# Performance work log

Hardware: AMD Instinct MI355X
Metric: run time of the kernel (lower is better)

## Reference

```python
import jax, jax.numpy as jnp
import numpy as np

B, L, N, C, H, COND = 2, 8, 256, 1024, 16, 64
D = C // H  # 64, divisible by 4


def setup_inputs() -> dict:
    key = jax.random.key(0)
    ks = jax.random.split(key, 16)
    w = lambda k, i, o: (jax.random.normal(k, (i, o), jnp.float32) / np.sqrt(i)).astype(jnp.float32)
    return {
        "s_frames": jax.random.normal(ks[0], (B, L, N, C), jnp.float32),
        "frame_idx": jnp.arange(L, dtype=jnp.int32),
        "seq_idx": jnp.sort(jax.random.randint(ks[1], (B, N), 0, 1024), axis=-1).astype(jnp.int32),
        "mask": jax.random.randint(ks[2], (B, L, N), 0, 2).astype(jnp.int32),
        "cond": jax.random.normal(ks[3], (B, COND), jnp.float32),
        "W_ada": w(ks[4], COND, 2 * C), "b_ada": jnp.zeros((2 * C,), jnp.float32),
        "Wq": w(ks[5], C, C), "bq": jnp.zeros((C,), jnp.float32),
        "Wk": w(ks[6], C, C), "bk": jnp.zeros((C,), jnp.float32),
        "Wv": w(ks[7], C, C), "bv": jnp.zeros((C,), jnp.float32),
        "Wo": w(ks[8], C, C), "bo": jnp.zeros((C,), jnp.float32),
    }


def _rope2d(x, pos_s, pos_f, inv_freq):
    # x: [B,H,T,D]; first half of D rotated by residue positions, second half by frame positions.
    half = x.shape[-1] // 2
    quarter = half // 2

    def rot(xh, pos):  # xh [B,H,T,half], pos [B,T]
        ang = pos[:, None, :, None] * inv_freq  # [B,1,T,quarter]
        c, s = jnp.cos(ang), jnp.sin(ang)
        x1, x2 = xh[..., :quarter], xh[..., quarter:]
        return jnp.concatenate([x1 * c - x2 * s, x1 * s + x2 * c], axis=-1)

    return jnp.concatenate([rot(x[..., :half], pos_s), rot(x[..., half:], pos_f)], axis=-1)


def reference(s_frames, frame_idx, seq_idx, mask, cond,
              W_ada, b_ada, Wq, bq, Wk, bk, Wv, bv, Wo, bo):
    Bx, Lx, Nx, Cx = s_frames.shape
    T = Lx * Nx
    Dh = Cx // H
    scale = Dh ** (-0.5)

    # AdaLN: LayerNorm (no affine) then conditional scale/shift from cond
    mu = s_frames.mean(-1, keepdims=True)
    var = ((s_frames - mu) ** 2).mean(-1, keepdims=True)
    xn = (s_frames - mu) * jax.lax.rsqrt(var + 1e-5)
    ss = cond @ W_ada + b_ada                      # [B, 2C]
    shift, sc = ss[:, :Cx], ss[:, Cx:]
    x = xn * (1.0 + sc[:, None, None, :]) + shift[:, None, None, :]

    xf = x.reshape(Bx, T, Cx)
    split = lambda t: t.reshape(Bx, T, H, Dh).transpose(0, 2, 1, 3)  # [B,H,T,D]
    q = split(xf @ Wq + bq)
    k = split(xf @ Wk + bk)
    v = split(xf @ Wv + bv)

    # 2D RoPE positions (token t = l*N + n)
    half = Dh // 2
    quarter = half // 2
    inv_freq = 1.0 / (10000.0 ** (jnp.arange(quarter, dtype=jnp.float32) * 2.0 / half))
    pos_s = jnp.tile(seq_idx, (1, Lx)).astype(jnp.float32)                                  # [B,T]
    pos_f = jnp.broadcast_to(jnp.repeat(frame_idx, Nx).astype(jnp.float32)[None], (Bx, T))  # [B,T]
    q = _rope2d(q, pos_s, pos_f, inv_freq)
    k = _rope2d(k, pos_s, pos_f, inv_freq)

    # additive bias: block-causal over frames + key padding mask
    fi = jnp.repeat(jnp.arange(Lx), Nx)                      # [T]
    future = fi[None, :] > fi[:, None]                       # [T,T] key frame > query frame
    bias = jnp.where(future, -jnp.inf, 0.0)[None, None]      # [1,1,T,T]
    pad = (mask.reshape(Bx, T) == 0)
    bias = jnp.where(pad[:, None, None, :], -jnp.inf, bias)  # [B,1,T,T]

    logits = jnp.einsum('bhtd,bhsd->bhts', q, k) * scale + bias
    w = jax.nn.softmax(logits, axis=-1)
    out = jnp.einsum('bhts,bhsd->bhtd', w, v)
    out = out.transpose(0, 2, 1, 3).reshape(Bx, Lx, Nx, Cx)
    return out @ Wo + bo
```

## Files before the change

kernel.cpp:

```cpp
#include <hip/hip_runtime.h>

typedef __bf16 bf16;
typedef __bf16 bf16x8 __attribute__((ext_vector_type(8)));
typedef __bf16 bf16x4 __attribute__((ext_vector_type(4)));
typedef float  f32x4  __attribute__((ext_vector_type(4)));

#define B_ 2
#define L_ 8
#define N_ 256
#define C_ 1024
#define H_ 16
#define D_ 64
#define T_ 2048
#define M_ 4096
#define COND_ 64

#define QSCALE 0.18033688011111372f

__device__ __forceinline__ void gload_lds16(const void* g, void* lds) {
  __builtin_amdgcn_global_load_lds((const __attribute__((address_space(1))) void*)g,
                                   (__attribute__((address_space(3))) void*)lds, 16, 0, 0);
}

__global__ __launch_bounds__(256) void k_ada(const float* __restrict__ cond,
                                             const float* __restrict__ W,
                                             const float* __restrict__ ba,
                                             float* __restrict__ ss) {
  int j = blockIdx.x * 256 + threadIdx.x;
  int b = j >> 11;
  int n = j & 2047;
  float s = ba[n];
  #pragma unroll
  for (int i = 0; i < COND_; ++i) s += cond[b * COND_ + i] * W[i * 2048 + n];
  ss[j] = s;
}

__global__ __launch_bounds__(256) void k_wt(const float* __restrict__ Wq,
                                            const float* __restrict__ Wk,
                                            const float* __restrict__ Wv,
                                            const float* __restrict__ Wo,
                                            bf16* __restrict__ Wt) {
  __shared__ float lds[64][65];
  int z = blockIdx.z;
  const float* W = (z == 0) ? Wq : (z == 1) ? Wk : (z == 2) ? Wv : Wo;
  int k0 = blockIdx.y * 64, n0 = blockIdx.x * 64;
  int tid = threadIdx.x;
  int r = tid >> 4, c4 = (tid & 15) * 4;
  #pragma unroll
  for (int p = 0; p < 4; ++p) {
    float4 v = *(const float4*)&W[(size_t)(k0 + p * 16 + r) * 1024 + n0 + c4];
    lds[p * 16 + r][c4] = v.x; lds[p * 16 + r][c4 + 1] = v.y;
    lds[p * 16 + r][c4 + 2] = v.z; lds[p * 16 + r][c4 + 3] = v.w;
  }
  __syncthreads();
  #pragma unroll
  for (int p = 0; p < 4; ++p) {
    int j = p * 16 + r;
    int i0 = c4;
    bf16x4 o;
    o[0] = (bf16)lds[i0][j]; o[1] = (bf16)lds[i0 + 1][j];
    o[2] = (bf16)lds[i0 + 2][j]; o[3] = (bf16)lds[i0 + 3][j];
    *(bf16x4*)&Wt[(size_t)(z * 1024 + n0 + j) * 1024 + k0 + i0] = o;
  }
}

__global__ __launch_bounds__(256) void k_ln(const float* __restrict__ x,
                                            const float* __restrict__ ss,
                                            bf16* __restrict__ xo) {
  int row = blockIdx.x;
  int b = row >> 11;
  int tid = threadIdx.x;
  float4 v = *(const float4*)&x[(size_t)row * 1024 + tid * 4];
  float s = v.x + v.y + v.z + v.w;
  float s2 = v.x * v.x + v.y * v.y + v.z * v.z + v.w * v.w;
  #pragma unroll
  for (int o = 32; o > 0; o >>= 1) { s += __shfl_down(s, o); s2 += __shfl_down(s2, o); }
  __shared__ float rs[4], rs2[4];
  int w = tid >> 6, l = tid & 63;
  if (l == 0) { rs[w] = s; rs2[w] = s2; }
  __syncthreads();
  s = rs[0] + rs[1] + rs[2] + rs[3];
  s2 = rs2[0] + rs2[1] + rs2[2] + rs2[3];
  float mu = s * (1.f / 1024.f);
  float var = s2 * (1.f / 1024.f) - mu * mu;
  float rinv = rsqrtf(var + 1e-5f);
  int c = tid * 4;
  float4 sh = *(const float4*)&ss[b * 2048 + c];
  float4 sc = *(const float4*)&ss[b * 2048 + 1024 + c];
  bf16x4 o;
  o[0] = (bf16)((v.x - mu) * rinv * (1.f + sc.x) + sh.x);
  o[1] = (bf16)((v.y - mu) * rinv * (1.f + sc.y) + sh.y);
  o[2] = (bf16)((v.z - mu) * rinv * (1.f + sc.z) + sh.z);
  o[3] = (bf16)((v.w - mu) * rinv * (1.f + sc.w) + sh.w);
  *(bf16x4*)&xo[(size_t)row * 1024 + c] = o;
}

template <int OUTBF>
__global__ __launch_bounds__(256) void k_gemm(const bf16* __restrict__ A,
                                              const bf16* __restrict__ Bt,
                                              const float* __restrict__ bi0,
                                              const float* __restrict__ bi1,
                                              const float* __restrict__ bi2,
                                              void* __restrict__ outp,
                                              int Nn, int K) {
  __shared__ __attribute__((aligned(16))) bf16 As[128 * 32];
  __shared__ __attribute__((aligned(16))) bf16 Bs[128 * 32];
  int n0 = blockIdx.x * 128, m0 = blockIdx.y * 128;
  int tid = threadIdx.x;
  int w = tid >> 6, l = tid & 63, cc = l & 15, g = l >> 4;
  int wm = w >> 1, wn = w & 1;
  f32x4 acc[4][4] = {};
  const bf16* Ag = A + (size_t)(m0 + (tid >> 2)) * K + (tid & 3) * 8;
  const bf16* Bg = Bt + (size_t)(n0 + (tid >> 2)) * K + (tid & 3) * 8;
  bf16* Adst = As + w * 16 * 32;
  bf16* Bdst = Bs + w * 16 * 32;
  int nk = K >> 5;
  for (int kt = 0; kt < nk; ++kt) {
    gload_lds16(Ag + kt * 32, Adst);
    gload_lds16(Ag + kt * 32 + (size_t)64 * K, Adst + 64 * 32);
    gload_lds16(Bg + kt * 32, Bdst);
    gload_lds16(Bg + kt * 32 + (size_t)64 * K, Bdst + 64 * 32);
    __syncthreads();
    bf16x8 a[4], bb[4];
    #pragma unroll
    for (int mi = 0; mi < 4; ++mi) a[mi] = *(const bf16x8*)&As[(wm * 64 + mi * 16 + cc) * 32 + g * 8];
    #pragma unroll
    for (int ni = 0; ni < 4; ++ni) bb[ni] = *(const bf16x8*)&Bs[(wn * 64 + ni * 16 + cc) * 32 + g * 8];
    #pragma unroll
    for (int mi = 0; mi < 4; ++mi)
      #pragma unroll
      for (int ni = 0; ni < 4; ++ni)
        acc[mi][ni] = __builtin_amdgcn_mfma_f32_16x16x32_bf16(a[mi], bb[ni], acc[mi][ni], 0, 0, 0);
    __syncthreads();
  }
  #pragma unroll
  for (int mi = 0; mi < 4; ++mi) {
    #pragma unroll
    for (int ni = 0; ni < 4; ++ni) {
      int col = n0 + wn * 64 + ni * 16 + cc;
      float bias = (col < 1024) ? bi0[col] : (col < 2048) ? bi1[col - 1024] : bi2[col - 2048];
      #pragma unroll
      for (int r = 0; r < 4; ++r) {
        int row = m0 + wm * 64 + mi * 16 + g * 4 + r;
        float v = acc[mi][ni][r] + bias;
        if (OUTBF) ((bf16*)outp)[(size_t)row * Nn + col] = (bf16)v;
        else       ((float*)outp)[(size_t)row * Nn + col] = v;
      }
    }
  }
}

__global__ __launch_bounds__(256) void k_rope(bf16* __restrict__ qkv,
                                              const int* __restrict__ seq_idx,
                                              const int* __restrict__ frame_idx) {
  int row = blockIdx.x;
  int b = row >> 11, t = row & 2047;
  float pos_s = (float)seq_idx[b * N_ + (t & 255)];
  float pos_f = (float)frame_idx[t >> 8];
  int tid = threadIdx.x;
  #pragma unroll
  for (int it = 0; it < 4; ++it) {
    int which = it * 256 + tid;
    int qk = which >> 9;
    int rem = which & 511;
    int h = rem >> 5;
    int half = (rem >> 4) & 1;
    int j = rem & 15;
    size_t base = (size_t)row * 3072 + qk * 1024 + h * 64 + half * 32;
    float x1 = (float)qkv[base + j];
    float x2 = (float)qkv[base + 16 + j];
    float pos = half ? pos_f : pos_s;
    float invf = exp2f(-0.8304820237218405f * (float)j);
    float ang = pos * invf;
    float sn, cs;
    sincosf(ang, &sn, &cs);
    float o1 = x1 * cs - x2 * sn;
    float o2 = x1 * sn + x2 * cs;
    float scl = (qk == 0) ? QSCALE : 1.0f;
    qkv[base + j] = (bf16)(o1 * scl);
    qkv[base + 16 + j] = (bf16)(o2 * scl);
  }
}

__global__ __launch_bounds__(256) void k_vt(const bf16* __restrict__ qkv, bf16* __restrict__ vt) {
  __shared__ __attribute__((aligned(16))) bf16 lds[64][72];
  int t0 = blockIdx.x * 64;
  int h = blockIdx.y, b = blockIdx.z;
  int tid = threadIdx.x;
  int i = tid >> 2, j0 = (tid & 3) * 16;
  const bf16* src = qkv + (size_t)(b * T_ + t0 + i) * 3072 + 2048 + h * 64 + j0;
  *(bf16x8*)&lds[i][j0] = *(const bf16x8*)src;
  *(bf16x8*)&lds[i][j0 + 8] = *(const bf16x8*)(src + 8);
  __syncthreads();
  int j = tid >> 2, i0 = (tid & 3) * 16;
  bf16x8 o0, o1;
  #pragma unroll
  for (int u = 0; u < 8; ++u) { o0[u] = lds[i0 + u][j]; o1[u] = lds[i0 + 8 + u][j]; }
  bf16* dst = vt + ((size_t)(b * H_ + h) * 64 + j) * T_ + t0 + i0;
  *(bf16x8*)dst = o0;
  *(bf16x8*)(dst + 8) = o1;
}

__global__ __launch_bounds__(256) void k_attn(const bf16* __restrict__ qkv,
                                              const bf16* __restrict__ vt,
                                              const int* __restrict__ mask,
                                              bf16* __restrict__ out) {
  __shared__ __attribute__((aligned(16))) bf16 Ks[2][64 * 64];
  __shared__ __attribute__((aligned(16))) bf16 Vs[2][64 * 64];
  __shared__ __attribute__((aligned(16))) bf16 Plds[4][16][72];
  __shared__ int Ms[2048];
  int wid = blockIdx.x;
  int f = 7 - (wid >> 7);
  int rem = wid & 127;
  int h = rem >> 3;
  int b = (rem >> 2) & 1;
  int tile = rem & 3;
  int t0 = f * 256 + tile * 64;
  int nchunk = (f + 1) * 4;
  int tid = threadIdx.x;
  int w = tid >> 6, l = tid & 63, cc = l & 15, g = l >> 4;

  int rbase = w * 16 + (l >> 3);
  int px = (l & 7) ^ (l >> 3);
  int ldst = w * 1024 + l * 8;

  int trow = t0 + w * 16 + cc;
  const bf16* qp = qkv + (size_t)((size_t)b * T_ + trow) * 3072 + h * 64;
  bf16x8 aq0 = *(const bf16x8*)(qp + g * 8);
  bf16x8 aq1 = *(const bf16x8*)(qp + 32 + g * 8);
  f32x4 o[4] = {};
  f32x4 o1 = {0.f, 0.f, 0.f, 0.f};
  float mrow[4] = {-1e30f, -1e30f, -1e30f, -1e30f};
  const int* mp = mask + b * T_;

  bf16x8 onesv;
  #pragma unroll
  for (int u = 0; u < 8; ++u) onesv[u] = (bf16)1.0f;

  #pragma unroll
  for (int j = 0; j < 2; ++j)
    gload_lds16(mp + w * 512 + j * 256 + l * 4, &Ms[w * 512 + j * 256 + l * 4]);

  #define STAGE(buf, s0_)                                                              \
    do {                                                                               \
      _Pragma("unroll")                                                                \
      for (int j = 0; j < 2; ++j) {                                                    \
        int r_ = rbase + j * 8;                                                        \
        gload_lds16(qkv + (size_t)((size_t)b * T_ + (s0_) + r_) * 3072 + 1024 + h * 64 + px * 8, \
                    &Ks[buf][ldst + j * 512]);                                         \
        gload_lds16(vt + (size_t)((size_t)(b * H_ + h) * 64 + r_) * T_ + (s0_) + px * 8, \
                    &Vs[buf][ldst + j * 512]);                                         \
      }                                                                                \
    } while (0)

  STAGE(0, 0);
  int sw1 = (g ^ (cc & 7)) * 8;
  int sw2 = ((g + 4) ^ (cc & 7)) * 8;
  for (int scn = 0; scn < nchunk; ++scn) {
    int s0 = scn * 64;
    int cur = scn & 1;
    if (scn + 1 < nchunk) {
      STAGE(cur ^ 1, s0 + 64);
      asm volatile("s_waitcnt vmcnt(4)" ::: "memory");
    } else {
      asm volatile("s_waitcnt vmcnt(0)" ::: "memory");
    }
    __builtin_amdgcn_s_barrier();
    asm volatile("" ::: "memory");
    float biasv[4];
    #pragma unroll
    for (int ni = 0; ni < 4; ++ni) biasv[ni] = Ms[s0 + ni * 16 + cc] ? 0.f : -1e30f;
    f32x4 sac[4];
    #pragma unroll
    for (int ni = 0; ni < 4; ++ni) {
      int r = ni * 16 + cc;
      bf16x8 b0 = *(const bf16x8*)&Ks[cur][r * 64 + sw1];
      bf16x8 b1 = *(const bf16x8*)&Ks[cur][r * 64 + sw2];
      f32x4 z = {0.f, 0.f, 0.f, 0.f};
      sac[ni] = __builtin_amdgcn_mfma_f32_16x16x32_bf16(aq0, b0, z, 0, 0, 0);
      sac[ni] = __builtin_amdgcn_mfma_f32_16x16x32_bf16(aq1, b1, sac[ni], 0, 0, 0);
      #pragma unroll
      for (int r4 = 0; r4 < 4; ++r4) sac[ni][r4] += biasv[ni];
    }
    float pmax[4];
    #pragma unroll
    for (int r = 0; r < 4; ++r)
      pmax[r] = fmaxf(fmaxf(sac[0][r], sac[1][r]), fmaxf(sac[2][r], sac[3][r]));
    float over = fmaxf(fmaxf(pmax[0] - mrow[0], pmax[1] - mrow[1]),
                       fmaxf(pmax[2] - mrow[2], pmax[3] - mrow[3]));
    if (__any(over > 8.0f)) {
      float alpha[4];
      #pragma unroll
      for (int r = 0; r < 4; ++r) {
        float mx = pmax[r];
        mx = fmaxf(mx, __shfl_xor(mx, 1));
        mx = fmaxf(mx, __shfl_xor(mx, 2));
        mx = fmaxf(mx, __shfl_xor(mx, 4));
        mx = fmaxf(mx, __shfl_xor(mx, 8));
        float mn = fmaxf(mrow[r], mx);
        alpha[r] = exp2f(mrow[r] - mn);
        mrow[r] = mn;
      }
      #pragma unroll
      for (int ni = 0; ni < 4; ++ni)
        #pragma unroll
        for (int r = 0; r < 4; ++r)
          o[ni][r] *= alpha[r];
      #pragma unroll
      for (int r = 0; r < 4; ++r) o1[r] *= alpha[r];
    }
    #pragma unroll
    for (int ni = 0; ni < 4; ++ni)
      #pragma unroll
      for (int r = 0; r < 4; ++r)
        sac[ni][r] = exp2f(sac[ni][r] - mrow[r]);
    #pragma unroll
    for (int ni = 0; ni < 4; ++ni)
      #pragma unroll
      for (int r = 0; r < 4; ++r)
        Plds[w][g * 4 + r][cc + ni * 16] = (bf16)sac[ni][r];
    asm volatile("s_waitcnt lgkmcnt(0)" ::: "memory");
    bf16x8 ap0 = *(const bf16x8*)&Plds[w][cc][g * 8];
    bf16x8 ap1 = *(const bf16x8*)&Plds[w][cc][32 + g * 8];
    #pragma unroll
    for (int ni = 0; ni < 4; ++ni) {
      int d = ni * 16 + cc;
      bf16x8 v0 = *(const bf16x8*)&Vs[cur][d * 64 + sw1];
      bf16x8 v1 = *(const bf16x8*)&Vs[cur][d * 64 + sw2];
      o[ni] = __builtin_amdgcn_mfma_f32_16x16x32_bf16(ap0, v0, o[ni], 0, 0, 0);
      o[ni] = __builtin_amdgcn_mfma_f32_16x16x32_bf16(ap1, v1, o[ni], 0, 0, 0);
    }
    o1 = __builtin_amdgcn_mfma_f32_16x16x32_bf16(ap0, onesv, o1, 0, 0, 0);
    o1 = __builtin_amdgcn_mfma_f32_16x16x32_bf16(ap1, onesv, o1, 0, 0, 0);
    __builtin_amdgcn_s_barrier();
    asm volatile("" ::: "memory");
  }
  float rl[4];
  #pragma unroll
  for (int r = 0; r < 4; ++r) rl[r] = 1.0f / o1[r];
  #pragma unroll
  for (int ni = 0; ni < 4; ++ni)
    #pragma unroll
    for (int r = 0; r < 4; ++r) {
      int t = t0 + w * 16 + g * 4 + r;
      out[(size_t)((size_t)b * T_ + t) * 1024 + h * 64 + ni * 16 + cc] = (bf16)(o[ni][r] * rl[r]);
    }
  #undef STAGE
}

extern "C" void kernel_launch(void* const* d_in, const int* in_sizes, int n_in,
                              void* d_out, int out_size, void* d_ws, size_t ws_size,
                              hipStream_t stream) {
  const float* s_frames = (const float*)d_in[0];
  const int* frame_idx  = (const int*)d_in[1];
  const int* seq_idx    = (const int*)d_in[2];
  const int* mask       = (const int*)d_in[3];
  const float* cond     = (const float*)d_in[4];
  const float* W_ada    = (const float*)d_in[5];
  const float* b_ada    = (const float*)d_in[6];
  const float* Wq       = (const float*)d_in[7];
  const float* bq       = (const float*)d_in[8];
  const float* Wk       = (const float*)d_in[9];
  const float* bk       = (const float*)d_in[10];
  const float* Wv       = (const float*)d_in[11];
  const float* bv       = (const float*)d_in[12];
  const float* Wo       = (const float*)d_in[13];
  const float* bo       = (const float*)d_in[14];
  float* out = (float*)d_out;

  char* ws = (char*)d_ws;
  float* ss = (float*)(ws);
  bf16* xb  = (bf16*)(ws + 16384);
  bf16* Wt  = (bf16*)(ws + 16384 + 8388608);
  bf16* qkv = (bf16*)(ws + 16384 + 2 * 8388608);
  bf16* vt  = (bf16*)(ws + 16384 + 2 * 8388608 + 25165824);
  bf16* att = (bf16*)(ws + 16384 + 3 * 8388608 + 25165824);

  k_ada<<<16, 256, 0, stream>>>(cond, W_ada, b_ada, ss);
  k_wt<<<dim3(16, 16, 4), 256, 0, stream>>>(Wq, Wk, Wv, Wo, Wt);
  k_ln<<<4096, 256, 0, stream>>>(s_frames, ss, xb);
  k_gemm<1><<<dim3(24, 32), 256, 0, stream>>>(xb, Wt, bq, bk, bv, qkv, 3072, 1024);
  k_rope<<<4096, 256, 0, stream>>>(qkv, seq_idx, frame_idx);
  k_vt<<<dim3(32, 16, 2), 256, 0, stream>>>(qkv, vt);
  k_attn<<<1024, 256, 0, stream>>>(qkv, vt, mask, att);
  k_gemm<0><<<dim3(8, 32), 256, 0, stream>>>(att, Wt + (size_t)3072 * 1024, bo, bo, bo, out, 1024, 1024);
}
```

Measured before the change: 156.0 us.

## Process two 16-row query tiles per wave in attention to reuse K/V loads

Each attention workgroup now handles 128 query rows instead of 64: every wave holds two 16-row query fragments and reuses each K/V tile from LDS for both. This halves the grid to 512 blocks and halves global K/V staging traffic per query. In exchange it roughly doubles accumulator registers, which may lower occupancy, and leaves fewer blocks for load balancing across the causal frame sizes.

```diff
diff --git a/kernel.cpp b/kernel.cpp
--- a/kernel.cpp
+++ b/kernel.cpp
@@ -210,12 +210,12 @@
   __shared__ __attribute__((aligned(16))) bf16 Plds[4][16][72];
   __shared__ int Ms[2048];
   int wid = blockIdx.x;
-  int f = 7 - (wid >> 7);
-  int rem = wid & 127;
-  int h = rem >> 3;
-  int b = (rem >> 2) & 1;
-  int tile = rem & 3;
-  int t0 = f * 256 + tile * 64;
+  int f = 7 - (wid >> 6);
+  int rem = wid & 63;
+  int h = rem >> 2;
+  int b = (rem >> 1) & 1;
+  int sub = rem & 1;
+  int t0 = f * 256 + sub * 128;
   int nchunk = (f + 1) * 4;
   int tid = threadIdx.x;
   int w = tid >> 6, l = tid & 63, cc = l & 15, g = l >> 4;
@@ -224,13 +224,20 @@
   int px = (l & 7) ^ (l >> 3);
   int ldst = w * 1024 + l * 8;
 
-  int trow = t0 + w * 16 + cc;
-  const bf16* qp = qkv + (size_t)((size_t)b * T_ + trow) * 3072 + h * 64;
-  bf16x8 aq0 = *(const bf16x8*)(qp + g * 8);
-  bf16x8 aq1 = *(const bf16x8*)(qp + 32 + g * 8);
-  f32x4 o[4] = {};
-  f32x4 o1 = {0.f, 0.f, 0.f, 0.f};
-  float mrow[4] = {-1e30f, -1e30f, -1e30f, -1e30f};
+  bf16x8 aq[2][2];
+  #pragma unroll
+  for (int u = 0; u < 2; ++u) {
+    const bf16* qp = qkv + (size_t)((size_t)b * T_ + t0 + w * 32 + u * 16 + cc) * 3072 + h * 64;
+    aq[u][0] = *(const bf16x8*)(qp + g * 8);
+    aq[u][1] = *(const bf16x8*)(qp + 32 + g * 8);
+  }
+  f32x4 o[2][4] = {};
+  f32x4 o1v[2] = {};
+  float mrow[2][4];
+  #pragma unroll
+  for (int u = 0; u < 2; ++u)
+    #pragma unroll
+    for (int r = 0; r < 4; ++r) mrow[u][r] = -1e30f;
   const int* mp = mask + b * T_;
 
   bf16x8 onesv;
@@ -270,81 +277,102 @@
     float biasv[4];
     #pragma unroll
     for (int ni = 0; ni < 4; ++ni) biasv[ni] = Ms[s0 + ni * 16 + cc] ? 0.f : -1e30f;
-    f32x4 sac[4];
+    f32x4 sac[2][4];
     #pragma unroll
     for (int ni = 0; ni < 4; ++ni) {
       int r = ni * 16 + cc;
       bf16x8 b0 = *(const bf16x8*)&Ks[cur][r * 64 + sw1];
       bf16x8 b1 = *(const bf16x8*)&Ks[cur][r * 64 + sw2];
-      f32x4 z = {0.f, 0.f, 0.f, 0.f};
-      sac[ni] = __builtin_amdgcn_mfma_f32_16x16x32_bf16(aq0, b0, z, 0, 0, 0);
-      sac[ni] = __builtin_amdgcn_mfma_f32_16x16x32_bf16(aq1, b1, sac[ni], 0, 0, 0);
-      #pragma unroll
-      for (int r4 = 0; r4 < 4; ++r4) sac[ni][r4] += biasv[ni];
+      #pragma unroll
+      for (int u = 0; u < 2; ++u) {
+        f32x4 z = {0.f, 0.f, 0.f, 0.f};
+        sac[u][ni] = __builtin_amdgcn_mfma_f32_16x16x32_bf16(aq[u][0], b0, z, 0, 0, 0);
+        sac[u][ni] = __builtin_amdgcn_mfma_f32_16x16x32_bf16(aq[u][1], b1, sac[u][ni], 0, 0, 0);
+        #pragma unroll
+        for (int r4 = 0; r4 < 4; ++r4) sac[u][ni][r4] += biasv[ni];
+      }
     }
-    float pmax[4];
-    #pragma unroll
-    for (int r = 0; r < 4; ++r)
-      pmax[r] = fmaxf(fmaxf(sac[0][r], sac[1][r]), fmaxf(sac[2][r], sac[3][r]));
-    float over = fmaxf(fmaxf(pmax[0] - mrow[0], pmax[1] - mrow[1]),
-                       fmaxf(pmax[2] - mrow[2], pmax[3] - mrow[3]));
+    float pmax[2][4];
+    #pragma unroll
+    for (int u = 0; u < 2; ++u)
+      #pragma unroll
+      for (int r = 0; r < 4; ++r)
+        pmax[u][r] = fmaxf(fmaxf(sac[u][0][r], sac[u][1][r]), fmaxf(sac[u][2][r], sac[u][3][r]));
+    float over = -1e30f;
+    #pragma unroll
+    for (int u = 0; u < 2; ++u)
+      #pragma unroll
+      for (int r = 0; r < 4; ++r)
+        over = fmaxf(over, pmax[u][r] - mrow[u][r]);
     if (__any(over > 8.0f)) {
-      float alpha[4];
-      #pragma unroll
-      for (int r = 0; r < 4; ++r) {
-        float mx = pmax[r];
-        mx = fmaxf(mx, __shfl_xor(mx, 1));
-        mx = fmaxf(mx, __shfl_xor(mx, 2));
-        mx = fmaxf(mx, __shfl_xor(mx, 4));
-        mx = fmaxf(mx, __shfl_xor(mx, 8));
-        float mn = fmaxf(mrow[r], mx);
-        alpha[r] = exp2f(mrow[r] - mn);
-        mrow[r] = mn;
+      #pragma unroll
+      for (int u = 0; u < 2; ++u) {
+        float alpha[4];
+        #pragma unroll
+        for (int r = 0; r < 4; ++r) {
+          float mx = pmax[u][r];
+          mx = fmaxf(mx, __shfl_xor(mx, 1));
+          mx = fmaxf(mx, __shfl_xor(mx, 2));
+          mx = fmaxf(mx, __shfl_xor(mx, 4));
+          mx = fmaxf(mx, __shfl_xor(mx, 8));
+          float mn = fmaxf(mrow[u][r], mx);
+          alpha[r] = exp2f(mrow[u][r] - mn);
+          mrow[u][r] = mn;
+        }
+        #pragma unroll
+        for (int ni = 0; ni < 4; ++ni)
+          #pragma unroll
+          for (int r = 0; r < 4; ++r)
+            o[u][ni][r] *= alpha[r];
+        #pragma unroll
+        for (int r = 0; r < 4; ++r) o1v[u][r] *= alpha[r];
       }
+    }
+    #pragma unroll
+    for (int u = 0; u < 2; ++u)
       #pragma unroll
       for (int ni = 0; ni < 4; ++ni)
         #pragma unroll
         for (int r = 0; r < 4; ++r)
-          o[ni][r] *= alpha[r];
-      #pragma unroll
-      for (int r = 0; r < 4; ++r) o1[r] *= alpha[r];
+          sac[u][ni][r] = exp2f(sac[u][ni][r] - mrow[u][r]);
+    #pragma unroll
+    for (int u = 0; u < 2; ++u) {
+      #pragma unroll
+      for (int ni = 0; ni < 4; ++ni)
+        #pragma unroll
+        for (int r = 0; r < 4; ++r)
+          Plds[w][g * 4 + r][cc + ni * 16] = (bf16)sac[u][ni][r];
+      asm volatile("s_waitcnt lgkmcnt(0)" ::: "memory");
+      bf16x8 ap0 = *(const bf16x8*)&Plds[w][cc][g * 8];
+      bf16x8 ap1 = *(const bf16x8*)&Plds[w][cc][32 + g * 8];
+      #pragma unroll
+      for (int ni = 0; ni < 4; ++ni) {
+        int d = ni * 16 + cc;
+        bf16x8 v0 = *(const bf16x8*)&Vs[cur][d * 64 + sw1];
+        bf16x8 v1 = *(const bf16x8*)&Vs[cur][d * 64 + sw2];
+        o[u][ni] = __builtin_amdgcn_mfma_f32_16x16x32_bf16(ap0, v0, o[u][ni], 0, 0, 0);
+        o[u][ni] = __builtin_amdgcn_mfma_f32_16x16x32_bf16(ap1, v1, o[u][ni], 0, 0, 0);
+      }
+      o1v[u] = __builtin_amdgcn_mfma_f32_16x16x32_bf16(ap0, onesv, o1v[u], 0, 0, 0);
+      o1v[u] = __builtin_amdgcn_mfma_f32_16x16x32_bf16(ap1, onesv, o1v[u], 0, 0, 0);
+      asm volatile("s_waitcnt lgkmcnt(0)" ::: "memory");
     }
-    #pragma unroll
-    for (int ni = 0; ni < 4; ++ni)
-      #pragma unroll
-      for (int r = 0; r < 4; ++r)
-        sac[ni][r] = exp2f(sac[ni][r] - mrow[r]);
-    #pragma unroll
-    for (int ni = 0; ni < 4; ++ni)
-      #pragma unroll
-      for (int r = 0; r < 4; ++r)
-        Plds[w][g * 4 + r][cc + ni * 16] = (bf16)sac[ni][r];
-    asm volatile("s_waitcnt lgkmcnt(0)" ::: "memory");
-    bf16x8 ap0 = *(const bf16x8*)&Plds[w][cc][g * 8];
-    bf16x8 ap1 = *(const bf16x8*)&Plds[w][cc][32 + g * 8];
-    #pragma unroll
-    for (int ni = 0; ni < 4; ++ni) {
-      int d = ni * 16 + cc;
-      bf16x8 v0 = *(const bf16x8*)&Vs[cur][d * 64 + sw1];
-      bf16x8 v1 = *(const bf16x8*)&Vs[cur][d * 64 + sw2];
-      o[ni] = __builtin_amdgcn_mfma_f32_16x16x32_bf16(ap0, v0, o[ni], 0, 0, 0);
-      o[ni] = __builtin_amdgcn_mfma_f32_16x16x32_bf16(ap1, v1, o[ni], 0, 0, 0);
-    }
-    o1 = __builtin_amdgcn_mfma_f32_16x16x32_bf16(ap0, onesv, o1, 0, 0, 0);
-    o1 = __builtin_amdgcn_mfma_f32_16x16x32_bf16(ap1, onesv, o1, 0, 0, 0);
     __builtin_amdgcn_s_barrier();
     asm volatile("" ::: "memory");
   }
-  float rl[4];
-  #pragma unroll
-  for (int r = 0; r < 4; ++r) rl[r] = 1.0f / o1[r];
-  #pragma unroll
-  for (int ni = 0; ni < 4; ++ni)
-    #pragma unroll
-    for (int r = 0; r < 4; ++r) {
-      int t = t0 + w * 16 + g * 4 + r;
-      out[(size_t)((size_t)b * T_ + t) * 1024 + h * 64 + ni * 16 + cc] = (bf16)(o[ni][r] * rl[r]);
-    }
+  #pragma unroll
+  for (int u = 0; u < 2; ++u) {
+    float rl[4];
+    #pragma unroll
+    for (int r = 0; r < 4; ++r) rl[r] = 1.0f / o1v[u][r];
+    #pragma unroll
+    for (int ni = 0; ni < 4; ++ni)
+      #pragma unroll
+      for (int r = 0; r < 4; ++r) {
+        int t = t0 + w * 32 + u * 16 + g * 4 + r;
+        out[(size_t)((size_t)b * T_ + t) * 1024 + h * 64 + ni * 16 + cc] = (bf16)(o[u][ni][r] * rl[r]);
+      }
+  }
   #undef STAGE
 }
 
@@ -382,6 +410,6 @@
   k_gemm<1><<<dim3(24, 32), 256, 0, stream>>>(xb, Wt, bq, bk, bv, qkv, 3072, 1024);
   k_rope<<<4096, 256, 0, stream>>>(qkv, seq_idx, frame_idx);
   k_vt<<<dim3(32, 16, 2), 256, 0, stream>>>(qkv, vt);
-  k_attn<<<1024, 256, 0, stream>>>(qkv, vt, mask, att);
+  k_attn<<<512, 256, 0, stream>>>(qkv, vt, mask, att);
   k_gemm<0><<<dim3(8, 32), 256, 0, stream>>>(att, Wt + (size_t)3072 * 1024, bo, bo, bo, out, 1024, 1024);
 }
```

Measured after the change: 177.6 us. 1.14x slower.

## Fuse RoPE, Q scaling and V transpose into the QKV GEMM epilogue

Applied to the files above, without the earlier changes.

Adds a dedicated QKV GEMM whose epilogue applies bias, 2D RoPE and the Q softmax scale to the Q and K columns, and writes V straight into the transposed per-head layout. This drops the separate rope and V-transpose kernels along with their read-modify-write passes over the 25 MB qkv buffer and two launches. In exchange the epilogue computes one sincos per accumulator row, and the V path writes transposed data in small 8-byte scattered chunks.

```diff
diff --git a/kernel.cpp b/kernel.cpp
--- a/kernel.cpp
+++ b/kernel.cpp
@@ -93,6 +93,101 @@
   o[2] = (bf16)((v.z - mu) * rinv * (1.f + sc.z) + sh.z);
   o[3] = (bf16)((v.w - mu) * rinv * (1.f + sc.w) + sh.w);
   *(bf16x4*)&xo[(size_t)row * 1024 + c] = o;
+}
+
+__global__ __launch_bounds__(256) void k_gemm_qkv(const bf16* __restrict__ A,
+                                                  const bf16* __restrict__ Bt,
+                                                  const float* __restrict__ bq,
+                                                  const float* __restrict__ bk,
+                                                  const float* __restrict__ bv,
+                                                  const int* __restrict__ seq_idx,
+                                                  const int* __restrict__ frame_idx,
+                                                  bf16* __restrict__ qkv,
+                                                  bf16* __restrict__ vt) {
+  __shared__ __attribute__((aligned(16))) bf16 As[128 * 32];
+  __shared__ __attribute__((aligned(16))) bf16 Bs[128 * 32];
+  const int K = 1024;
+  int n0 = blockIdx.x * 128, m0 = blockIdx.y * 128;
+  int tid = threadIdx.x;
+  int w = tid >> 6, l = tid & 63, cc = l & 15, g = l >> 4;
+  int wm = w >> 1, wn = w & 1;
+  f32x4 acc[4][4] = {};
+  const bf16* Ag = A + (size_t)(m0 + (tid >> 2)) * K + (tid & 3) * 8;
+  const bf16* Bg = Bt + (size_t)(n0 + (tid >> 2)) * K + (tid & 3) * 8;
+  bf16* Adst = As + w * 16 * 32;
+  bf16* Bdst = Bs + w * 16 * 32;
+  for (int kt = 0; kt < 32; ++kt) {
+    gload_lds16(Ag + kt * 32, Adst);
+    gload_lds16(Ag + kt * 32 + (size_t)64 * K, Adst + 64 * 32);
+    gload_lds16(Bg + kt * 32, Bdst);
+    gload_lds16(Bg + kt * 32 + (size_t)64 * K, Bdst + 64 * 32);
+    __syncthreads();
+    bf16x8 a[4], bb[4];
+    #pragma unroll
+    for (int mi = 0; mi < 4; ++mi) a[mi] = *(const bf16x8*)&As[(wm * 64 + mi * 16 + cc) * 32 + g * 8];
+    #pragma unroll
+    for (int ni = 0; ni < 4; ++ni) bb[ni] = *(const bf16x8*)&Bs[(wn * 64 + ni * 16 + cc) * 32 + g * 8];
+    #pragma unroll
+    for (int mi = 0; mi < 4; ++mi)
+      #pragma unroll
+      for (int ni = 0; ni < 4; ++ni)
+        acc[mi][ni] = __builtin_amdgcn_mfma_f32_16x16x32_bf16(a[mi], bb[ni], acc[mi][ni], 0, 0, 0);
+    __syncthreads();
+  }
+  int region = blockIdx.x >> 3;
+  const float* bp = (region == 0) ? bq : (region == 1) ? bk : bv;
+  int b = m0 >> 11;
+  if (region < 2) {
+    float* Ps = (float*)As;
+    if (tid < 128) Ps[tid] = (float)seq_idx[b * 256 + (m0 & 255) + tid];
+    __syncthreads();
+    float invf = exp2f(-0.8304820237218405f * (float)cc);
+    float posf = (float)frame_idx[(m0 & 2047) >> 8];
+    float snf, csf;
+    sincosf(posf * invf, &snf, &csf);
+    float scl = (region == 0) ? QSCALE : 1.0f;
+    csf *= scl; snf *= scl;
+    int colbase = n0 + wn * 64 + cc;
+    float b0 = bp[colbase & 1023];
+    float b1 = bp[(colbase + 16) & 1023];
+    float b2 = bp[(colbase + 32) & 1023];
+    float b3 = bp[(colbase + 48) & 1023];
+    #pragma unroll
+    for (int mi = 0; mi < 4; ++mi) {
+      #pragma unroll
+      for (int r = 0; r < 4; ++r) {
+        int lr = wm * 64 + mi * 16 + g * 4 + r;
+        float sns, css;
+        sincosf(Ps[lr] * invf, &sns, &css);
+        css *= scl; sns *= scl;
+        float x0 = acc[mi][0][r] + b0;
+        float x1 = acc[mi][1][r] + b1;
+        float x2 = acc[mi][2][r] + b2;
+        float x3 = acc[mi][3][r] + b3;
+        bf16* op = qkv + (size_t)(m0 + lr) * 3072 + colbase;
+        op[0]  = (bf16)(x0 * css - x1 * sns);
+        op[16] = (bf16)(x0 * sns + x1 * css);
+        op[32] = (bf16)(x2 * csf - x3 * snf);
+        op[48] = (bf16)(x2 * snf + x3 * csf);
+      }
+    }
+  } else {
+    int h = (blockIdx.x - 16) * 2 + wn;
+    int tbase = (m0 & 2047) + wm * 64;
+    #pragma unroll
+    for (int ni = 0; ni < 4; ++ni) {
+      int d = ni * 16 + cc;
+      float bias = bp[h * 64 + d];
+      #pragma unroll
+      for (int mi = 0; mi < 4; ++mi) {
+        bf16x4 pk;
+        #pragma unroll
+        for (int r = 0; r < 4; ++r) pk[r] = (bf16)(acc[mi][ni][r] + bias);
+        int t = tbase + mi * 16 + g * 4;
+        *(bf16x4*)&vt[((size_t)(b * 16 + h) * 64 + d) * 2048 + t] = pk;
+      }
+    }
+  }
 }
 
 template <int OUTBF>
@@ -150,57 +245,6 @@
   }
 }
 
-__global__ __launch_bounds__(256) void k_rope(bf16* __restrict__ qkv,
-                                              const int* __restrict__ seq_idx,
-                                              const int* __restrict__ frame_idx) {
-  int row = blockIdx.x;
-  int b = row >> 11, t = row & 2047;
-  float pos_s = (float)seq_idx[b * N_ + (t & 255)];
-  float pos_f = (float)frame_idx[t >> 8];
-  int tid = threadIdx.x;
-  #pragma unroll
-  for (int it = 0; it < 4; ++it) {
-    int which = it * 256 + tid;
-    int qk = which >> 9;
-    int rem = which & 511;
-    int h = rem >> 5;
-    int half = (rem >> 4) & 1;
-    int j = rem & 15;
-    size_t base = (size_t)row * 3072 + qk * 1024 + h * 64 + half * 32;
-    float x1 = (float)qkv[base + j];
-    float x2 = (float)qkv[base + 16 + j];
-    float pos = half ? pos_f : pos_s;
-    float invf = exp2f(-0.8304820237218405f * (float)j);
-    float ang = pos * invf;
-    float sn, cs;
-    sincosf(ang, &sn, &cs);
-    float o1 = x1 * cs - x2 * sn;
-    float o2 = x1 * sn + x2 * cs;
-    float scl = (qk == 0) ? QSCALE : 1.0f;
-    qkv[base + j] = (bf16)(o1 * scl);
-    qkv[base + 16 + j] = (bf16)(o2 * scl);
-  }
-}
-
-__global__ __launch_bounds__(256) void k_vt(const bf16* __restrict__ qkv, bf16* __restrict__ vt) {
-  __shared__ __attribute__((aligned(16))) bf16 lds[64][72];
-  int t0 = blockIdx.x * 64;
-  int h = blockIdx.y, b = blockIdx.z;
-  int tid = threadIdx.x;
-  int i = tid >> 2, j0 = (tid & 3) * 16;
-  const bf16* src = qkv + (size_t)(b * T_ + t0 + i) * 3072 + 2048 + h * 64 + j0;
-  *(bf16x8*)&lds[i][j0] = *(const bf16x8*)src;
-  *(bf16x8*)&lds[i][j0 + 8] = *(const bf16x8*)(src + 8);
-  __syncthreads();
-  int j = tid >> 2, i0 = (tid & 3) * 16;
-  bf16x8 o0, o1;
-  #pragma unroll
-  for (int u = 0; u < 8; ++u) { o0[u] = lds[i0 + u][j]; o1[u] = lds[i0 + 8 + u][j]; }
-  bf16* dst = vt + ((size_t)(b * H_ + h) * 64 + j) * T_ + t0 + i0;
-  *(bf16x8*)dst = o0;
-  *(bf16x8*)(dst + 8) = o1;
-}
-
 __global__ __launch_bounds__(256) void k_attn(const bf16* __restrict__ qkv,
                                               const bf16* __restrict__ vt,
                                               const int* __restrict__ mask,
@@ -379,9 +423,7 @@
   k_ada<<<16, 256, 0, stream>>>(cond, W_ada, b_ada, ss);
   k_wt<<<dim3(16, 16, 4), 256, 0, stream>>>(Wq, Wk, Wv, Wo, Wt);
   k_ln<<<4096, 256, 0, stream>>>(s_frames, ss, xb);
-  k_gemm<1><<<dim3(24, 32), 256, 0, stream>>>(xb, Wt, bq, bk, bv, qkv, 3072, 1024);
-  k_rope<<<4096, 256, 0, stream>>>(qkv, seq_idx, frame_idx);
-  k_vt<<<dim3(32, 16, 2), 256, 0, stream>>>(qkv, vt);
+  k_gemm_qkv<<<dim3(24, 32), 256, 0, stream>>>(xb, Wt, bq, bk, bv, seq_idx, frame_idx, qkv, vt);
   k_attn<<<1024, 256, 0, stream>>>(qkv, vt, mask, att);
   k_gemm<0><<<dim3(8, 32), 256, 0, stream>>>(att, Wt + (size_t)3072 * 1024, bo, bo, bo, out, 1024, 1024);
 }
```

Result: no change. 153.1 us (-1.9%).
